# Kernel tuning notes

Hardware: AMD Instinct MI355X
Metric: run time of the kernel (lower is better)

The kernel has to match this reference:

```python
import jax, jax.numpy as jnp
import numpy as np

HEADS = 8  # from init_kwargs

def setup_inputs() -> dict:
    key = jax.random.key(0)
    ks = jax.random.split(key, 7)
    B, C, H, W = 8, 256, 128, 128
    s = 1.0 / np.sqrt(C).astype(np.float32)
    return {
        "x": jax.random.normal(ks[0], (B, C, H, W), jnp.float32),
        "context": jax.random.normal(ks[1], (B, C, H, W), jnp.float32),
        "Wq": jax.random.normal(ks[2], (C, C), jnp.float32) * s,
        "Wkv": jax.random.normal(ks[3], (2 * C, C), jnp.float32) * s,
        "Wout": jax.random.normal(ks[4], (C, C), jnp.float32) * s,
        "Wscale": jax.random.normal(ks[5], (C, C), jnp.float32) * s,
        "Wshift": jax.random.normal(ks[6], (C, C), jnp.float32) * s,
    }

def reference(x, context, Wq, Wkv, Wout, Wscale, Wshift):
    B, C, H, W = x.shape
    h = HEADS
    e = C // h
    # mode='row': faithful raw reshape (NOT a permute), exactly as the torch code does
    xr = x.reshape(-1, W, C)        # [B*H, W, C] in raw row-major layout
    ctx = context.reshape(-1, W, C)
    q = xr @ Wq.T                   # nn.Linear: x @ W.T
    kv = xr @ Wkv.T
    k, v = kv[..., :C], kv[..., C:]
    scale = ctx @ Wscale.T
    shift = ctx @ Wshift.T
    # FiLM modulation on q, k, v
    q = scale * q + shift
    k = scale * k + shift
    v = scale * v + shift
    b = q.shape[0]
    split = lambda t: t.reshape(b, -1, h, e).transpose(0, 2, 1, 3)  # [b, h, t, e]
    qh, kh, vh = split(q), split(k), split(v)
    dots = jnp.einsum('bhie,bhje->bhij', qh, kh) * (e ** -0.5)
    attn = jax.nn.softmax(dots, axis=-1)
    out = jnp.einsum('bhij,bhje->bhie', attn, vh)    # [b, h, t, e]
    out = out.transpose(0, 2, 1, 3).reshape(b, -1, C)
    out = out @ Wout.T
    return out.reshape(B, C, H, W)
```

## Files before the change

kernel.cpp:

```cpp
#include <hip/hip_runtime.h>
#include <cstdint>

typedef short bf8 __attribute__((ext_vector_type(8)));
typedef float f4  __attribute__((ext_vector_type(4)));
typedef uint32_t u32x4 __attribute__((ext_vector_type(4)));
typedef unsigned short u16;

__device__ __forceinline__ u16 f2bf(float f) {
  union { float f; uint32_t u; } v; v.f = f;
  uint32_t u = v.u + 0x7fffu + ((v.u >> 16) & 1u);
  return (u16)(u >> 16);
}

__device__ __forceinline__ uint32_t pk2(float lo, float hi) {
  return (uint32_t)f2bf(lo) | ((uint32_t)f2bf(hi) << 16);
}

__device__ __forceinline__ bf8 ld_cvt8(const float* p) {
  f4 a = *(const f4*)p;
  f4 b = *(const f4*)(p + 4);
  u32x4 r;
  r[0] = pk2(a[0], a[1]);
  r[1] = pk2(a[2], a[3]);
  r[2] = pk2(b[0], b[1]);
  r[3] = pk2(b[2], b[3]);
  return __builtin_bit_cast(bf8, r);
}

#define MFMA(a, b, c) __builtin_amdgcn_mfma_f32_16x16x32_bf16((a), (b), (c), 0, 0, 0)

constexpr int SEQ = 128;
constexpr int CH  = 256;
constexpr int NH  = 8;

constexpr size_t OQ   = 0;
constexpr size_t OKV  = 65536;
constexpr size_t OOUT = 196608;
constexpr size_t OSC  = 262144;
constexpr size_t OSH  = 327680;
constexpr size_t W_ELEMS  = 393216;
constexpr size_t OH_ELEMS = (size_t)1024 * SEQ * CH;

__device__ constexpr size_t WOFF[10] = {
  OQ, OQ + 4096, OKV, OKV + 4096, OKV + 65536, OKV + 69632,
  OSC, OSC + 4096, OSH, OSH + 4096 };
__device__ constexpr int ROWADD[10] = {0, 16, 0, 16, 256, 272, 0, 16, 0, 16};

__global__ void cvt_weights(const float* __restrict__ wq, const float* __restrict__ wkv,
                            const float* __restrict__ wout, const float* __restrict__ wsc,
                            const float* __restrict__ wsh, u16* __restrict__ dst) {
  int i = (blockIdx.x * 256 + threadIdx.x) * 8;
  const float* s; int off;
  if      (i <  65536) { s = wq;   off = i; }
  else if (i < 196608) { s = wkv;  off = i -  65536; }
  else if (i < 262144) { s = wout; off = i - 196608; }
  else if (i < 327680) { s = wsc;  off = i - 262144; }
  else                 { s = wsh;  off = i - 327680; }
  *(bf8*)(dst + i) = ld_cvt8(s + off);
}

template<bool WB, bool SPLIT>
__global__ __launch_bounds__(256, SPLIT ? 3 : 2)
void fused_axattn(const float* __restrict__ x,   const float* __restrict__ ctx,
                  const u16* __restrict__ Wb,
                  const float* __restrict__ Wqf, const float* __restrict__ Wkvf,
                  const float* __restrict__ Wscf, const float* __restrict__ Wshf,
                  const float* __restrict__ Woutf,
                  u16* __restrict__ Oh, float* __restrict__ out)
{
  __shared__ u16 sQ[SEQ][40];
  __shared__ u16 sK[SEQ][40];
  __shared__ u16 sVT[32][136];
  __shared__ u16 sP[SEQ][40];

  const int tid  = threadIdx.x;
  const int wave = tid >> 6;
  const int lane = tid & 63;
  const int l15  = lane & 15;
  const int quad = lane >> 4;
  const int g    = blockIdx.x;
  const size_t gbase = (size_t)g * (SEQ * CH);
  const int ib = wave * 32;

  const float SCALE = 0.17677669529663687f;
  const int vo = l15 * CH + quad * 8;

  f4 pacc[2][16];
  if constexpr (!SPLIT) {
    #pragma unroll
    for (int mt = 0; mt < 2; ++mt)
      #pragma unroll
      for (int nt = 0; nt < 16; ++nt) pacc[mt][nt] = 0.0f;
  }

  for (int h = 0; h < NH; ++h) {
    const int hoff = h * 32 * CH;

    auto ldb = [&](int t, int cc) -> bf8 {
      if constexpr (WB) {
        return *(const bf8*)(Wb + WOFF[t] + hoff + vo + cc);
      } else {
        const float* base = (t < 2) ? Wqf : (t < 6) ? Wkvf : (t < 8) ? Wscf : Wshf;
        return ld_cvt8(base + (size_t)(h * 32 + ROWADD[t] + l15) * CH + quad * 8 + cc);
      }
    };

    #pragma unroll
    for (int mt = 0; mt < 2; ++mt) {
      f4 acc[10];
      #pragma unroll
      for (int t = 0; t < 10; ++t) acc[t] = 0.0f;

      const float* xrow = x   + gbase + (size_t)(ib + 16 * mt + l15) * CH + quad * 8;
      const float* crow = ctx + gbase + (size_t)(ib + 16 * mt + l15) * CH + quad * 8;

      #pragma unroll
      for (int kc = 0; kc < 8; ++kc) {
        const int cc = kc * 32;
        bf8 ax = ld_cvt8(xrow + cc);
        bf8 ac = ld_cvt8(crow + cc);
        #pragma unroll
        for (int t = 0; t < 10; ++t)
          acc[t] = MFMA((t < 6) ? ax : ac, ldb(t, cc), acc[t]);
      }

      #pragma unroll
      for (int r = 0; r < 4; ++r) {
        const int i = ib + 16 * mt + 4 * quad + r;
        const float sc0 = acc[6][r], sc1 = acc[7][r];
        const float sh0 = acc[8][r], sh1 = acc[9][r];
        sQ[i][l15]      = f2bf(sc0 * acc[0][r] + sh0);
        sQ[i][16 + l15] = f2bf(sc1 * acc[1][r] + sh1);
        sK[i][l15]      = f2bf(sc0 * acc[2][r] + sh0);
        sK[i][16 + l15] = f2bf(sc1 * acc[3][r] + sh1);
        sVT[l15][i]      = f2bf(sc0 * acc[4][r] + sh0);
        sVT[16 + l15][i] = f2bf(sc1 * acc[5][r] + sh1);
      }
    }
    __syncthreads();

    #pragma unroll
    for (int mt = 0; mt < 2; ++mt) {
      const int i0 = ib + 16 * mt;
      bf8 aq = *(const bf8*)(&sQ[i0 + l15][quad * 8]);
      f4 sc[8];
      #pragma unroll
      for (int ct = 0; ct < 8; ++ct) {
        bf8 bk = *(const bf8*)(&sK[ct * 16 + l15][quad * 8]);
        f4 z = 0.0f;
        sc[ct] = MFMA(aq, bk, z);
      }

      float mx[4] = {-3.4e38f, -3.4e38f, -3.4e38f, -3.4e38f};
      #pragma unroll
      for (int ct = 0; ct < 8; ++ct)
        #pragma unroll
        for (int r = 0; r < 4; ++r) mx[r] = fmaxf(mx[r], sc[ct][r]);
      #pragma unroll
      for (int m = 1; m <= 8; m <<= 1)
        #pragma unroll
        for (int r = 0; r < 4; ++r) mx[r] = fmaxf(mx[r], __shfl_xor(mx[r], m));

      float sm[4] = {0.f, 0.f, 0.f, 0.f};
      #pragma unroll
      for (int ct = 0; ct < 8; ++ct)
        #pragma unroll
        for (int r = 0; r < 4; ++r) {
          float p = __expf((sc[ct][r] - mx[r]) * SCALE);
          sm[r] += p;
          sc[ct][r] = p;
        }
      #pragma unroll
      for (int m = 1; m <= 8; m <<= 1)
        #pragma unroll
        for (int r = 0; r < 4; ++r) sm[r] += __shfl_xor(sm[r], m);
      float rv[4];
      #pragma unroll
      for (int r = 0; r < 4; ++r) rv[r] = 1.0f / sm[r];

      f4 o0 = 0.0f, o1 = 0.0f;
      #pragma unroll
      for (int q = 0; q < 4; ++q) {
        #pragma unroll
        for (int c2 = 0; c2 < 2; ++c2) {
          const int ct = 2 * q + c2;
          #pragma unroll
          for (int r = 0; r < 4; ++r)
            sP[i0 + 4 * quad + r][c2 * 16 + l15] = f2bf(sc[ct][r]);
        }
        asm volatile("s_waitcnt lgkmcnt(0)" ::: "memory");
        bf8 ap  = *(const bf8*)(&sP[i0 + l15][quad * 8]);
        bf8 bv0 = *(const bf8*)(&sVT[l15][q * 32 + quad * 8]);
        bf8 bv1 = *(const bf8*)(&sVT[16 + l15][q * 32 + quad * 8]);
        o0 = MFMA(ap, bv0, o0);
        o1 = MFMA(ap, bv1, o1);
      }

      if constexpr (SPLIT) {
        #pragma unroll
        for (int r = 0; r < 4; ++r) {
          const size_t orow = gbase + (size_t)(i0 + 4 * quad + r) * CH + h * 32;
          Oh[orow + l15]      = f2bf(o0[r] * rv[r]);
          Oh[orow + 16 + l15] = f2bf(o1[r] * rv[r]);
        }
      } else {
        #pragma unroll
        for (int r = 0; r < 4; ++r) {
          sP[i0 + 4 * quad + r][l15]      = f2bf(o0[r] * rv[r]);
          sP[i0 + 4 * quad + r][16 + l15] = f2bf(o1[r] * rv[r]);
        }
      }
    }

    if constexpr (!SPLIT) {
      asm volatile("s_waitcnt lgkmcnt(0)" ::: "memory");
      bf8 a0 = *(const bf8*)(&sP[ib + l15][quad * 8]);
      bf8 a1 = *(const bf8*)(&sP[ib + 16 + l15][quad * 8]);
      #pragma unroll
      for (int nt = 0; nt < 16; ++nt) {
        bf8 b;
        if constexpr (WB) b = *(const bf8*)(Wb + OOUT + (size_t)(nt * 16 + l15) * CH + h * 32 + quad * 8);
        else              b = ld_cvt8(Woutf + (size_t)(nt * 16 + l15) * CH + h * 32 + quad * 8);
        pacc[0][nt] = MFMA(a0, b, pacc[0][nt]);
        pacc[1][nt] = MFMA(a1, b, pacc[1][nt]);
      }
    }
    __syncthreads();
  }

  if constexpr (!SPLIT) {
    #pragma unroll
    for (int mt = 0; mt < 2; ++mt)
      #pragma unroll
      for (int nt = 0; nt < 16; ++nt)
        #pragma unroll
        for (int r = 0; r < 4; ++r)
          out[gbase + (size_t)(ib + 16 * mt + 4 * quad + r) * CH + nt * 16 + l15] =
              pacc[mt][nt][r];
  }
}

__global__ __launch_bounds__(256, 2)
void proj_gemm(const u16* __restrict__ Oh, const u16* __restrict__ Wb,
               float* __restrict__ out)
{
  const int tid  = threadIdx.x;
  const int wave = tid >> 6;
  const int lane = tid & 63;
  const int l15  = lane & 15;
  const int quad = lane >> 4;
  const int g    = blockIdx.x;
  const size_t gbase = (size_t)g * (SEQ * CH);
  const int ib = wave * 32;

  f4 pacc[2][16];
  #pragma unroll
  for (int mt = 0; mt < 2; ++mt)
    #pragma unroll
    for (int nt = 0; nt < 16; ++nt) pacc[mt][nt] = 0.0f;

  const u16* arow = Oh + gbase + (size_t)(ib + l15) * CH + quad * 8;
  const u16* wrow = Wb + OOUT + (size_t)l15 * CH + quad * 8;

  #pragma unroll
  for (int kc = 0; kc < 8; ++kc) {
    const int cc = kc * 32;
    bf8 a0 = *(const bf8*)(arow + cc);
    bf8 a1 = *(const bf8*)(arow + 16 * CH + cc);
    #pragma unroll
    for (int nt = 0; nt < 16; ++nt) {
      bf8 b = *(const bf8*)(wrow + (size_t)nt * 16 * CH + cc);
      pacc[0][nt] = MFMA(a0, b, pacc[0][nt]);
      pacc[1][nt] = MFMA(a1, b, pacc[1][nt]);
    }
  }

  #pragma unroll
  for (int mt = 0; mt < 2; ++mt)
    #pragma unroll
    for (int nt = 0; nt < 16; ++nt)
      #pragma unroll
      for (int r = 0; r < 4; ++r)
        out[gbase + (size_t)(ib + 16 * mt + 4 * quad + r) * CH + nt * 16 + l15] =
            pacc[mt][nt][r];
}

extern "C" void kernel_launch(void* const* d_in, const int* in_sizes, int n_in,
                              void* d_out, int out_size, void* d_ws, size_t ws_size,
                              hipStream_t stream) {
  const float* x    = (const float*)d_in[0];
  const float* ctx  = (const float*)d_in[1];
  const float* Wq   = (const float*)d_in[2];
  const float* Wkv  = (const float*)d_in[3];
  const float* Wout = (const float*)d_in[4];
  const float* Wsc  = (const float*)d_in[5];
  const float* Wsh  = (const float*)d_in[6];
  float* o = (float*)d_out;

  const size_t need_w     = W_ELEMS * sizeof(u16);
  const size_t need_split = (W_ELEMS + OH_ELEMS) * sizeof(u16);

  if (ws_size >= need_split) {
    u16* w  = (u16*)d_ws;
    u16* oh = w + W_ELEMS;
    cvt_weights<<<dim3(192), dim3(256), 0, stream>>>(Wq, Wkv, Wout, Wsc, Wsh, w);
    fused_axattn<true, true><<<dim3(1024), dim3(256), 0, stream>>>(
        x, ctx, w, nullptr, nullptr, nullptr, nullptr, nullptr, oh, nullptr);
    proj_gemm<<<dim3(1024), dim3(256), 0, stream>>>(oh, w, o);
  } else if (ws_size >= need_w) {
    u16* w = (u16*)d_ws;
    cvt_weights<<<dim3(192), dim3(256), 0, stream>>>(Wq, Wkv, Wout, Wsc, Wsh, w);
    fused_axattn<true, false><<<dim3(1024), dim3(256), 0, stream>>>(
        x, ctx, w, nullptr, nullptr, nullptr, nullptr, nullptr, nullptr, o);
  } else {
    fused_axattn<false, false><<<dim3(1024), dim3(256), 0, stream>>>(
        x, ctx, nullptr, Wq, Wkv, Wsc, Wsh, Wout, nullptr, o);
  }
}
```

Before: 1.123 ms.

## Split fused attention into QKV-modulation, per-head attention, and projection kernels

```diff
diff --git a/kernel.cpp b/kernel.cpp
--- a/kernel.cpp
+++ b/kernel.cpp
@@ -32,14 +32,15 @@
 constexpr int SEQ = 128;
 constexpr int CH  = 256;
 constexpr int NH  = 8;
+constexpr int NG  = 1024;
 
 constexpr size_t OQ   = 0;
 constexpr size_t OKV  = 65536;
 constexpr size_t OOUT = 196608;
 constexpr size_t OSC  = 262144;
 constexpr size_t OSH  = 327680;
-constexpr size_t W_ELEMS  = 393216;
-constexpr size_t OH_ELEMS = (size_t)1024 * SEQ * CH;
+constexpr size_t W_ELEMS = 393216;
+constexpr size_t XE      = (size_t)NG * SEQ * CH;
 
 __device__ constexpr size_t WOFF[10] = {
   OQ, OQ + 4096, OKV, OKV + 4096, OKV + 65536, OKV + 69632,
@@ -59,20 +60,174 @@
   *(bf8*)(dst + i) = ld_cvt8(s + off);
 }
 
-template<bool WB, bool SPLIT>
-__global__ __launch_bounds__(256, SPLIT ? 3 : 2)
-void fused_axattn(const float* __restrict__ x,   const float* __restrict__ ctx,
-                  const u16* __restrict__ Wb,
-                  const float* __restrict__ Wqf, const float* __restrict__ Wkvf,
-                  const float* __restrict__ Wscf, const float* __restrict__ Wshf,
-                  const float* __restrict__ Woutf,
-                  u16* __restrict__ Oh, float* __restrict__ out)
+__global__ __launch_bounds__(256, 3)
+void qkvmod(const float* __restrict__ x, const float* __restrict__ ctx,
+            const u16* __restrict__ Wb,
+            u16* __restrict__ Qm, u16* __restrict__ Km, u16* __restrict__ VmT)
 {
-  __shared__ u16 sQ[SEQ][40];
+  __shared__ u16 sVT[2][32][72];
+
+  const int tid  = threadIdx.x;
+  const int wave = tid >> 6;
+  const int lane = tid & 63;
+  const int l15  = lane & 15;
+  const int quad = lane >> 4;
+  const int g    = blockIdx.x >> 1;
+  const int half = blockIdx.x & 1;
+  const int i0   = half * 64 + wave * 16;
+  const size_t gbase = (size_t)g * (SEQ * CH);
+  const int vo = l15 * CH + quad * 8;
+
+  bf8 ax[8], ac[8];
+  {
+    const float* xr = x   + gbase + (size_t)(i0 + l15) * CH + quad * 8;
+    const float* cr = ctx + gbase + (size_t)(i0 + l15) * CH + quad * 8;
+    #pragma unroll
+    for (int kc = 0; kc < 8; ++kc) { ax[kc] = ld_cvt8(xr + kc * 32); ac[kc] = ld_cvt8(cr + kc * 32); }
+  }
+
+  for (int h = 0; h < NH; ++h) {
+    const int hoff = h * 32 * CH;
+    f4 acc[10];
+    #pragma unroll
+    for (int t = 0; t < 10; ++t) acc[t] = 0.0f;
+
+    #pragma unroll
+    for (int kc = 0; kc < 8; ++kc) {
+      const int cc = kc * 32;
+      #pragma unroll
+      for (int t = 0; t < 10; ++t) {
+        bf8 b = *(const bf8*)(Wb + WOFF[t] + hoff + vo + cc);
+        acc[t] = MFMA((t < 6) ? ax[kc] : ac[kc], b, acc[t]);
+      }
+    }
+
+    #pragma unroll
+    for (int r = 0; r < 4; ++r) {
+      const int i  = i0 + 4 * quad + r;
+      const int il = i - half * 64;
+      const float sc0 = acc[6][r], sc1 = acc[7][r];
+      const float sh0 = acc[8][r], sh1 = acc[9][r];
+      const size_t orow = gbase + (size_t)i * CH + h * 32;
+      Qm[orow + l15]      = f2bf(sc0 * acc[0][r] + sh0);
+      Qm[orow + 16 + l15] = f2bf(sc1 * acc[1][r] + sh1);
+      Km[orow + l15]      = f2bf(sc0 * acc[2][r] + sh0);
+      Km[orow + 16 + l15] = f2bf(sc1 * acc[3][r] + sh1);
+      sVT[h & 1][l15][il]      = f2bf(sc0 * acc[4][r] + sh0);
+      sVT[h & 1][16 + l15][il] = f2bf(sc1 * acc[5][r] + sh1);
+    }
+    __syncthreads();
+    {
+      const int d = tid >> 3, c8 = (tid & 7) * 8;
+      bf8 v = *(const bf8*)(&sVT[h & 1][d][c8]);
+      *(bf8*)(VmT + ((size_t)(g * NH + h) * 32 + d) * SEQ + half * 64 + c8) = v;
+    }
+  }
+}
+
+__global__ __launch_bounds__(256, 4)
+void attn_heads(u16* Qm, const u16* __restrict__ Km, const u16* __restrict__ VmT)
+{
   __shared__ u16 sK[SEQ][40];
   __shared__ u16 sVT[32][136];
   __shared__ u16 sP[SEQ][40];
 
+  const int tid  = threadIdx.x;
+  const int wave = tid >> 6;
+  const int lane = tid & 63;
+  const int l15  = lane & 15;
+  const int quad = lane >> 4;
+  const int g    = blockIdx.x >> 3;
+  const int h    = blockIdx.x & 7;
+  const size_t gbase = (size_t)g * (SEQ * CH);
+  const int ib = wave * 32;
+
+  const float SCALE = 0.17677669529663687f;
+
+  #pragma unroll
+  for (int it = 0; it < 2; ++it) {
+    int idx = tid + it * 256;
+    int j = idx >> 2, c = (idx & 3) * 8;
+    *(bf8*)(&sK[j][c]) = *(const bf8*)(Km + gbase + (size_t)j * CH + h * 32 + c);
+  }
+  #pragma unroll
+  for (int it = 0; it < 2; ++it) {
+    int idx = tid + it * 256;
+    int d = idx >> 4, c = (idx & 15) * 8;
+    *(bf8*)(&sVT[d][c]) = *(const bf8*)(VmT + ((size_t)(g * NH + h) * 32 + d) * SEQ + c);
+  }
+  __syncthreads();
+
+  #pragma unroll
+  for (int mt = 0; mt < 2; ++mt) {
+    const int i0 = ib + 16 * mt;
+    bf8 aq = *(const bf8*)(Qm + gbase + (size_t)(i0 + l15) * CH + h * 32 + quad * 8);
+    f4 sc[8];
+    #pragma unroll
+    for (int ct = 0; ct < 8; ++ct) {
+      bf8 bk = *(const bf8*)(&sK[ct * 16 + l15][quad * 8]);
+      f4 z = 0.0f;
+      sc[ct] = MFMA(aq, bk, z);
+    }
+
+    float mx[4] = {-3.4e38f, -3.4e38f, -3.4e38f, -3.4e38f};
+    #pragma unroll
+    for (int ct = 0; ct < 8; ++ct)
+      #pragma unroll
+      for (int r = 0; r < 4; ++r) mx[r] = fmaxf(mx[r], sc[ct][r]);
+    #pragma unroll
+    for (int m = 1; m <= 8; m <<= 1)
+      #pragma unroll
+      for (int r = 0; r < 4; ++r) mx[r] = fmaxf(mx[r], __shfl_xor(mx[r], m));
+
+    float sm[4] = {0.f, 0.f, 0.f, 0.f};
+    #pragma unroll
+    for (int ct = 0; ct < 8; ++ct)
+      #pragma unroll
+      for (int r = 0; r < 4; ++r) {
+        float p = __expf((sc[ct][r] - mx[r]) * SCALE);
+        sm[r] += p;
+        sc[ct][r] = p;
+      }
+    #pragma unroll
+    for (int m = 1; m <= 8; m <<= 1)
+      #pragma unroll
+      for (int r = 0; r < 4; ++r) sm[r] += __shfl_xor(sm[r], m);
+    float rv[4];
+    #pragma unroll
+    for (int r = 0; r < 4; ++r) rv[r] = 1.0f / sm[r];
+
+    f4 o0 = 0.0f, o1 = 0.0f;
+    #pragma unroll
+    for (int q = 0; q < 4; ++q) {
+      #pragma unroll
+      for (int c2 = 0; c2 < 2; ++c2) {
+        const int ct = 2 * q + c2;
+        #pragma unroll
+        for (int r = 0; r < 4; ++r)
+          sP[i0 + 4 * quad + r][c2 * 16 + l15] = f2bf(sc[ct][r]);
+      }
+      asm volatile("s_waitcnt lgkmcnt(0)" ::: "memory");
+      bf8 ap  = *(const bf8*)(&sP[i0 + l15][quad * 8]);
+      bf8 bv0 = *(const bf8*)(&sVT[l15][q * 32 + quad * 8]);
+      bf8 bv1 = *(const bf8*)(&sVT[16 + l15][q * 32 + quad * 8]);
+      o0 = MFMA(ap, bv0, o0);
+      o1 = MFMA(ap, bv1, o1);
+    }
+
+    #pragma unroll
+    for (int r = 0; r < 4; ++r) {
+      const size_t orow = gbase + (size_t)(i0 + 4 * quad + r) * CH + h * 32;
+      Qm[orow + l15]      = f2bf(o0[r] * rv[r]);
+      Qm[orow + 16 + l15] = f2bf(o1[r] * rv[r]);
+    }
+  }
+}
+
+__global__ __launch_bounds__(256, 2)
+void proj_gemm(const u16* __restrict__ Oh, const u16* __restrict__ Wb,
+               float* __restrict__ out)
+{
   const int tid  = threadIdx.x;
   const int wave = tid >> 6;
   const int lane = tid & 63;
@@ -82,20 +237,71 @@
   const size_t gbase = (size_t)g * (SEQ * CH);
   const int ib = wave * 32;
 
+  f4 pacc[2][16];
+  #pragma unroll
+  for (int mt = 0; mt < 2; ++mt)
+    #pragma unroll
+    for (int nt = 0; nt < 16; ++nt) pacc[mt][nt] = 0.0f;
+
+  const u16* arow = Oh + gbase + (size_t)(ib + l15) * CH + quad * 8;
+  const u16* wrow = Wb + OOUT + (size_t)l15 * CH + quad * 8;
+
+  #pragma unroll
+  for (int kc = 0; kc < 8; ++kc) {
+    const int cc = kc * 32;
+    bf8 a0 = *(const bf8*)(arow + cc);
+    bf8 a1 = *(const bf8*)(arow + 16 * CH + cc);
+    #pragma unroll
+    for (int nt = 0; nt < 16; ++nt) {
+      bf8 b = *(const bf8*)(wrow + (size_t)nt * 16 * CH + cc);
+      pacc[0][nt] = MFMA(a0, b, pacc[0][nt]);
+      pacc[1][nt] = MFMA(a1, b, pacc[1][nt]);
+    }
+  }
+
+  #pragma unroll
+  for (int mt = 0; mt < 2; ++mt)
+    #pragma unroll
+    for (int nt = 0; nt < 16; ++nt)
+      #pragma unroll
+      for (int r = 0; r < 4; ++r)
+        out[gbase + (size_t)(ib + 16 * mt + 4 * quad + r) * CH + nt * 16 + l15] =
+            pacc[mt][nt][r];
+}
+
+template<bool WB>
+__global__ __launch_bounds__(256, 2)
+void fused_axattn(const float* __restrict__ x,   const float* __restrict__ ctx,
+                  const u16* __restrict__ Wb,
+                  const float* __restrict__ Wqf, const float* __restrict__ Wkvf,
+                  const float* __restrict__ Wscf, const float* __restrict__ Wshf,
+                  const float* __restrict__ Woutf, float* __restrict__ out)
+{
+  __shared__ u16 sQ[SEQ][40];
+  __shared__ u16 sK[SEQ][40];
+  __shared__ u16 sVT[32][136];
+  __shared__ u16 sP[SEQ][40];
+
+  const int tid  = threadIdx.x;
+  const int wave = tid >> 6;
+  const int lane = tid & 63;
+  const int l15  = lane & 15;
+  const int quad = lane >> 4;
+  const int g    = blockIdx.x;
+  const size_t gbase = (size_t)g * (SEQ * CH);
+  const int ib = wave * 32;
+
   const float SCALE = 0.17677669529663687f;
   const int vo = l15 * CH + quad * 8;
 
   f4 pacc[2][16];
-  if constexpr (!SPLIT) {
-    #pragma unroll
-    for (int mt = 0; mt < 2; ++mt)
-      #pragma unroll
-      for (int nt = 0; nt < 16; ++nt) pacc[mt][nt] = 0.0f;
-  }
+  #pragma unroll
+  for (int mt = 0; mt < 2; ++mt)
+    #pragma unroll
+    for (int nt = 0; nt < 16; ++nt) pacc[mt][nt] = 0.0f;
 
   for (int h = 0; h < NH; ++h) {
     const int hoff = h * 32 * CH;
-
     auto ldb = [&](int t, int cc) -> bf8 {
       if constexpr (WB) {
         return *(const bf8*)(Wb + WOFF[t] + hoff + vo + cc);
@@ -110,20 +316,17 @@
       f4 acc[10];
       #pragma unroll
       for (int t = 0; t < 10; ++t) acc[t] = 0.0f;
-
       const float* xrow = x   + gbase + (size_t)(ib + 16 * mt + l15) * CH + quad * 8;
       const float* crow = ctx + gbase + (size_t)(ib + 16 * mt + l15) * CH + quad * 8;
-
       #pragma unroll
       for (int kc = 0; kc < 8; ++kc) {
         const int cc = kc * 32;
-        bf8 ax = ld_cvt8(xrow + cc);
-        bf8 ac = ld_cvt8(crow + cc);
+        bf8 axx = ld_cvt8(xrow + cc);
+        bf8 acc2 = ld_cvt8(crow + cc);
         #pragma unroll
         for (int t = 0; t < 10; ++t)
-          acc[t] = MFMA((t < 6) ? ax : ac, ldb(t, cc), acc[t]);
-      }
-
+          acc[t] = MFMA((t < 6) ? axx : acc2, ldb(t, cc), acc[t]);
+      }
       #pragma unroll
       for (int r = 0; r < 4; ++r) {
         const int i = ib + 16 * mt + 4 * quad + r;
@@ -150,7 +353,6 @@
         f4 z = 0.0f;
         sc[ct] = MFMA(aq, bk, z);
       }
-
       float mx[4] = {-3.4e38f, -3.4e38f, -3.4e38f, -3.4e38f};
       #pragma unroll
       for (int ct = 0; ct < 8; ++ct)
@@ -160,7 +362,6 @@
       for (int m = 1; m <= 8; m <<= 1)
         #pragma unroll
         for (int r = 0; r < 4; ++r) mx[r] = fmaxf(mx[r], __shfl_xor(mx[r], m));
-
       float sm[4] = {0.f, 0.f, 0.f, 0.f};
       #pragma unroll
       for (int ct = 0; ct < 8; ++ct)
@@ -195,25 +396,15 @@
         o0 = MFMA(ap, bv0, o0);
         o1 = MFMA(ap, bv1, o1);
       }
-
-      if constexpr (SPLIT) {
-        #pragma unroll
-        for (int r = 0; r < 4; ++r) {
-          const size_t orow = gbase + (size_t)(i0 + 4 * quad + r) * CH + h * 32;
-          Oh[orow + l15]      = f2bf(o0[r] * rv[r]);
-          Oh[orow + 16 + l15] = f2bf(o1[r] * rv[r]);
-        }
-      } else {
-        #pragma unroll
-        for (int r = 0; r < 4; ++r) {
-          sP[i0 + 4 * quad + r][l15]      = f2bf(o0[r] * rv[r]);
-          sP[i0 + 4 * quad + r][16 + l15] = f2bf(o1[r] * rv[r]);
-        }
-      }
-    }
-
-    if constexpr (!SPLIT) {
-      asm volatile("s_waitcnt lgkmcnt(0)" ::: "memory");
+      #pragma unroll
+      for (int r = 0; r < 4; ++r) {
+        sP[i0 + 4 * quad + r][l15]      = f2bf(o0[r] * rv[r]);
+        sP[i0 + 4 * quad + r][16 + l15] = f2bf(o1[r] * rv[r]);
+      }
+    }
+
+    asm volatile("s_waitcnt lgkmcnt(0)" ::: "memory");
+    {
       bf8 a0 = *(const bf8*)(&sP[ib + l15][quad * 8]);
       bf8 a1 = *(const bf8*)(&sP[ib + 16 + l15][quad * 8]);
       #pragma unroll
@@ -226,53 +417,6 @@
       }
     }
     __syncthreads();
-  }
-
-  if constexpr (!SPLIT) {
-    #pragma unroll
-    for (int mt = 0; mt < 2; ++mt)
-      #pragma unroll
-      for (int nt = 0; nt < 16; ++nt)
-        #pragma unroll
-        for (int r = 0; r < 4; ++r)
-          out[gbase + (size_t)(ib + 16 * mt + 4 * quad + r) * CH + nt * 16 + l15] =
-              pacc[mt][nt][r];
-  }
-}
-
-__global__ __launch_bounds__(256, 2)
-void proj_gemm(const u16* __restrict__ Oh, const u16* __restrict__ Wb,
-               float* __restrict__ out)
-{
-  const int tid  = threadIdx.x;
-  const int wave = tid >> 6;
-  const int lane = tid & 63;
-  const int l15  = lane & 15;
-  const int quad = lane >> 4;
-  const int g    = blockIdx.x;
-  const size_t gbase = (size_t)g * (SEQ * CH);
-  const int ib = wave * 32;
-
-  f4 pacc[2][16];
-  #pragma unroll
-  for (int mt = 0; mt < 2; ++mt)
-    #pragma unroll
-    for (int nt = 0; nt < 16; ++nt) pacc[mt][nt] = 0.0f;
-
-  const u16* arow = Oh + gbase + (size_t)(ib + l15) * CH + quad * 8;
-  const u16* wrow = Wb + OOUT + (size_t)l15 * CH + quad * 8;
-
-  #pragma unroll
-  for (int kc = 0; kc < 8; ++kc) {
-    const int cc = kc * 32;
-    bf8 a0 = *(const bf8*)(arow + cc);
-    bf8 a1 = *(const bf8*)(arow + 16 * CH + cc);
-    #pragma unroll
-    for (int nt = 0; nt < 16; ++nt) {
-      bf8 b = *(const bf8*)(wrow + (size_t)nt * 16 * CH + cc);
-      pacc[0][nt] = MFMA(a0, b, pacc[0][nt]);
-      pacc[1][nt] = MFMA(a1, b, pacc[1][nt]);
-    }
   }
 
   #pragma unroll
@@ -297,23 +441,25 @@
   const float* Wsh  = (const float*)d_in[6];
   float* o = (float*)d_out;
 
-  const size_t need_w     = W_ELEMS * sizeof(u16);
-  const size_t need_split = (W_ELEMS + OH_ELEMS) * sizeof(u16);
-
-  if (ws_size >= need_split) {
-    u16* w  = (u16*)d_ws;
-    u16* oh = w + W_ELEMS;
+  const size_t need_w    = W_ELEMS * sizeof(u16);
+  const size_t need_pipe = (W_ELEMS + 3 * XE) * sizeof(u16);
+
+  if (ws_size >= need_pipe) {
+    u16* w   = (u16*)d_ws;
+    u16* qm  = w + W_ELEMS;
+    u16* km  = qm + XE;
+    u16* vmt = km + XE;
     cvt_weights<<<dim3(192), dim3(256), 0, stream>>>(Wq, Wkv, Wout, Wsc, Wsh, w);
-    fused_axattn<true, true><<<dim3(1024), dim3(256), 0, stream>>>(
-        x, ctx, w, nullptr, nullptr, nullptr, nullptr, nullptr, oh, nullptr);
-    proj_gemm<<<dim3(1024), dim3(256), 0, stream>>>(oh, w, o);
+    qkvmod<<<dim3(2048), dim3(256), 0, stream>>>(x, ctx, w, qm, km, vmt);
+    attn_heads<<<dim3(8192), dim3(256), 0, stream>>>(qm, km, vmt);
+    proj_gemm<<<dim3(1024), dim3(256), 0, stream>>>(qm, w, o);
   } else if (ws_size >= need_w) {
     u16* w = (u16*)d_ws;
     cvt_weights<<<dim3(192), dim3(256), 0, stream>>>(Wq, Wkv, Wout, Wsc, Wsh, w);
-    fused_axattn<true, false><<<dim3(1024), dim3(256), 0, stream>>>(
-        x, ctx, w, nullptr, nullptr, nullptr, nullptr, nullptr, nullptr, o);
+    fused_axattn<true><<<dim3(1024), dim3(256), 0, stream>>>(
+        x, ctx, w, nullptr, nullptr, nullptr, nullptr, nullptr, o);
   } else {
-    fused_axattn<false, false><<<dim3(1024), dim3(256), 0, stream>>>(
-        x, ctx, nullptr, Wq, Wkv, Wsc, Wsh, Wout, nullptr, o);
-  }
-}
+    fused_axattn<false><<<dim3(1024), dim3(256), 0, stream>>>(
+        x, ctx, nullptr, Wq, Wkv, Wsc, Wsh, Wout, o);
+  }
+}
```

New measurement: 1.014 ms. 9.7% less time.
